# Kernel optimization log

Measured on AMD Instinct MI355X. Metric: run time of the kernel, lower is better.

Reference implementation:

```python
import jax, jax.numpy as jnp
import numpy as np


def setup_inputs() -> dict:
    key = jax.random.key(0)
    ks = jax.random.split(key, 8)
    B, W, H, C = 4, 64, 64, 256
    C2 = C // 2
    s = 0.05
    x = jax.random.normal(ks[0], (B, W, H, C), dtype=jnp.float32)
    Wq = jax.random.normal(ks[1], (C, C2), dtype=jnp.float32) * s
    bq = jax.random.normal(ks[2], (C2,), dtype=jnp.float32) * s
    Wk = jax.random.normal(ks[3], (C, C2), dtype=jnp.float32) * s
    bk = jax.random.normal(ks[4], (C2,), dtype=jnp.float32) * s
    Wv = jax.random.normal(ks[5], (C, C), dtype=jnp.float32) * s
    bv = jax.random.normal(ks[6], (C,), dtype=jnp.float32) * s
    # gamma is initialized to 0 in the original; use a nonzero value so the
    # attention branch actually contributes (math is identical).
    gamma = jnp.array([0.5], dtype=jnp.float32)
    return {"x": x, "Wq": Wq, "bq": bq, "Wk": Wk, "bk": bk, "Wv": Wv, "bv": bv, "gamma": gamma}


def reference(x, Wq, bq, Wk, bk, Wv, bv, gamma):
    B, W, H, C = x.shape
    N = W * H
    # 1x1 convs == per-pixel linear projections
    q = jnp.einsum('bwhc,cd->bwhd', x, Wq) + bq   # [B,W,H,C/2]
    k = jnp.einsum('bwhc,cd->bwhd', x, Wk) + bk   # [B,W,H,C/2]
    v = jnp.einsum('bwhc,cd->bwhd', x, Wv) + bv   # [B,W,H,C]
    # Faithful to original: raw row-major reshape (B,W,H,Cq) -> (B,Cq,N)
    # (this mixes spatial and channel axes, exactly as the TF code does)
    pq = q.reshape(B, -1, N)                      # [B,C/2,N]
    pk = k.reshape(B, -1, N)                      # [B,C/2,N]
    pv = v.reshape(B, -1, N)                      # [B,C,N]
    energy = jnp.einsum('bcn,bcm->bnm', pq, pk)   # [B,N,N] (pq transposed)
    attention = jax.nn.softmax(energy, axis=-1)   # [B,N,N]
    out = jnp.einsum('bcm,bnm->bcn', pv, attention)  # pv @ attention^T
    out = out.reshape(B, W, H, C)
    return gamma * out + x
```

## Files before the change

kernel.cpp:

```cpp
#include <hip/hip_runtime.h>
#include <hip/hip_bf16.h>
#include <stdint.h>


typedef __attribute__((ext_vector_type(8)))  short short8;
typedef __attribute__((ext_vector_type(4)))  float f32x4;
typedef __attribute__((ext_vector_type(16))) float f32x16;
typedef __attribute__((ext_vector_type(4)))  unsigned short u16x4;

#define MFMA16 __builtin_amdgcn_mfma_f32_16x16x32_bf16
#define MFMA32 __builtin_amdgcn_mfma_f32_32x32x16_bf16

__device__ __forceinline__ unsigned short f2bf(float f) {
    union { float f; uint32_t u; } v; v.f = f;
    return (unsigned short)((v.u + 0x8000u) >> 16);
}
__device__ __forceinline__ float bf2f(unsigned short h) {
    union { uint32_t u; float f; } v; v.u = ((uint32_t)h) << 16;
    return v.f;
}
__device__ __forceinline__ uint32_t pkbf(float a, float b) {
    union { __hip_bfloat162 h; uint32_t u; } v;
    v.h = __float22bfloat162_rn(float2{a, b});
    return v.u;
}

__global__ void prep_w(const float* __restrict__ Wq, const float* __restrict__ bq,
                       const float* __restrict__ Wk, const float* __restrict__ bk,
                       const float* __restrict__ Wv, const float* __restrict__ bv,
                       unsigned short* __restrict__ Wt, float* __restrict__ bias) {
    int g = blockIdx.x * 256 + threadIdx.x;
    int c = g & 255, d = g >> 8;
    float val;
    if (d < 128)      val = Wq[c * 128 + d];
    else if (d < 256) val = Wk[c * 128 + (d - 128)];
    else              val = Wv[c * 256 + (d - 256)];
    Wt[d * 256 + c] = f2bf(val);
    if (g < 512) {
        float bb;
        if (g < 128)      bb = bq[g];
        else if (g < 256) bb = bk[g - 128];
        else              bb = bv[g - 256];
        bias[g] = bb;
    }
}

__global__ __launch_bounds__(256) void proj(
        const float* __restrict__ x, const unsigned short* __restrict__ Wt,
        const float* __restrict__ bias,
        unsigned short* __restrict__ Qrm, unsigned short* __restrict__ Krm,
        unsigned short* __restrict__ Vbf) {
    __shared__ unsigned short T[128 * 136];
    int bid = blockIdx.x;
    int tid = threadIdx.x;
    int wave = tid >> 6, lane = tid & 63;
    int l16 = lane & 15, quad = lane >> 4;

    int kind, b, a, vh = 0;
    if (bid < 256) { kind = bid >> 7; int s = bid & 127; b = s >> 5; a = s & 31; }
    else           { kind = 2; int s = bid - 256; vh = s >> 7; b = (s >> 5) & 3; a = s & 31; }

    short8 af[2][8];
    #pragma unroll
    for (int g = 0; g < 2; ++g) {
        int p_local = wave * 32 + g * 16 + l16;
        int pix = (kind == 2) ? (b * 4096 + a * 128 + p_local)
                              : (b * 4096 + a + 32 * p_local);
        const float* xr = x + (size_t)pix * 256;
        #pragma unroll
        for (int kk = 0; kk < 8; ++kk) {
            f32x4 u0 = *(const f32x4*)(xr + kk * 32 + quad * 8);
            f32x4 u1 = *(const f32x4*)(xr + kk * 32 + quad * 8 + 4);
            union { short8 s; uint32_t u[4]; } h;
            h.u[0] = pkbf(u0[0], u0[1]); h.u[1] = pkbf(u0[2], u0[3]);
            h.u[2] = pkbf(u1[0], u1[1]); h.u[3] = pkbf(u1[2], u1[3]);
            af[g][kk] = h.s;
        }
    }

    if (kind < 2) {
        int dbase = kind * 128;
        unsigned short* out = kind ? Krm : Qrm;
        #pragma unroll 1
        for (int dt = 0; dt < 8; ++dt) {
            int d = dbase + dt * 16 + l16;
            float bval = bias[d];
            f32x4 acc0 = {0.f,0.f,0.f,0.f}, acc1 = {0.f,0.f,0.f,0.f};
            #pragma unroll
            for (int kk = 0; kk < 8; ++kk) {
                short8 wrow = *(const short8*)(Wt + d * 256 + kk * 32 + quad * 8);
                acc0 = MFMA16(af[0][kk], wrow, acc0, 0, 0, 0);
                acc1 = MFMA16(af[1][kk], wrow, acc1, 0, 0, 0);
            }
            #pragma unroll
            for (int g = 0; g < 2; ++g) {
                f32x4 acc = g ? acc1 : acc0;
                union { u16x4 v; uint32_t u[2]; } pk;
                pk.u[0] = pkbf(acc[0] + bval, acc[1] + bval);
                pk.u[1] = pkbf(acc[2] + bval, acc[3] + bval);
                *(u16x4*)(T + (dt * 16 + l16) * 136 + wave * 32 + g * 16 + quad * 4) = pk.v;
            }
        }
        __syncthreads();
        unsigned short* ob = out + (b << 19) + a * 128 * 128;
        #pragma unroll
        for (int it = 0; it < 8; ++it) {
            int ci = it * 256 + tid;
            int row = ci >> 4, cj = ci & 15;
            *(short8*)(ob + row * 128 + cj * 8) = *(const short8*)(T + row * 136 + cj * 8);
        }
    } else {
        #pragma unroll 1
        for (int dt = 0; dt < 8; ++dt) {
            int d = 256 + vh * 128 + dt * 16 + l16;
            f32x4 acc0 = {0.f,0.f,0.f,0.f}, acc1 = {0.f,0.f,0.f,0.f};
            #pragma unroll
            for (int kk = 0; kk < 8; ++kk) {
                short8 wrow = *(const short8*)(Wt + d * 256 + kk * 32 + quad * 8);
                acc0 = MFMA16(wrow, af[0][kk], acc0, 0, 0, 0);
                acc1 = MFMA16(wrow, af[1][kk], acc1, 0, 0, 0);
            }
            int dvl = dt * 16 + quad * 4;
            f32x4 bv4 = *(const f32x4*)(bias + 256 + vh * 128 + dvl);
            #pragma unroll
            for (int g = 0; g < 2; ++g) {
                f32x4 acc = g ? acc1 : acc0;
                union { u16x4 v; uint32_t u[2]; } pk;
                pk.u[0] = pkbf(acc[0] + bv4[0], acc[1] + bv4[1]);
                pk.u[1] = pkbf(acc[2] + bv4[2], acc[3] + bv4[3]);
                int p_local = wave * 32 + g * 16 + l16;
                *(u16x4*)(T + p_local * 136 + dvl) = pk.v;
            }
        }
        __syncthreads();
        #pragma unroll
        for (int it = 0; it < 8; ++it) {
            int cid = it * 256 + tid;
            int c_local = cid >> 8, w = cid & 255;
            int p_local = c_local * 16 + (w >> 4);
            int m = (w >> 4) * 256 + vh * 128 + (w & 15) * 8;
            *(short8*)(Vbf + (b << 20) + (size_t)(a * 8 + c_local) * 4096 + m)
                = *(const short8*)(T + p_local * 136 + (w & 15) * 8);
        }
    }
}

__global__ __launch_bounds__(256, 2) void attn(
        const unsigned short* __restrict__ Qrm, const unsigned short* __restrict__ Krm,
        const unsigned short* __restrict__ Vbf, unsigned short* __restrict__ Opart,
        float* __restrict__ Lpart) {
    __shared__ unsigned short Vs[256 * 72];
    __shared__ unsigned short Ps[64 * 72];

    int bid = blockIdx.x;
    int comb = bid & 7, qt = bid >> 3;
    int b = comb >> 1, ks = comb & 1;
    int tid = threadIdx.x, wave = tid >> 6, lane = tid & 63;
    int l32 = lane & 31, half = lane >> 5;
    int mt = wave & 1, nt = wave >> 1;

    const unsigned short* Qb = Qrm + (b << 19);
    const unsigned short* Kb = Krm + (b << 19);
    const unsigned short* Vb = Vbf + (b << 20);

    int q0 = qt * 64;

    short8 qf[8];
    {
        const unsigned short* qrow = Qb + (q0 + nt * 32 + l32) * 128 + half * 8;
        #pragma unroll
        for (int kk = 0; kk < 8; ++kk) qf[kk] = *(const short8*)(qrow + kk * 16);
    }

    f32x16 O[2][2];
    #pragma unroll
    for (int i = 0; i < 2; ++i)
        #pragma unroll
        for (int j = 0; j < 2; ++j)
            #pragma unroll
            for (int r = 0; r < 16; ++r) O[i][j][r] = 0.f;
    float l_run = 0.f;

    const int m_base = ks * 2048;
    int vrow = tid >> 3, vch = tid & 7;

    short8 vreg[8];
    #pragma unroll
    for (int i = 0; i < 8; ++i)
        vreg[i] = *(const short8*)(Vb + (size_t)(vrow + i * 32) * 4096 + m_base + vch * 8);
    short8 kf[8];
    {
        const unsigned short* krow = Kb + (m_base + mt * 32 + l32) * 128 + half * 8;
        #pragma unroll
        for (int kk = 0; kk < 8; ++kk) kf[kk] = *(const short8*)(krow + kk * 16);
    }

    #pragma unroll 1
    for (int kt = 0; kt < 32; ++kt) {
        __syncthreads();
        #pragma unroll
        for (int i = 0; i < 8; ++i)
            *(short8*)(Vs + (vrow + i * 32) * 72 + vch * 8) = vreg[i];

        f32x16 S;
        #pragma unroll
        for (int r = 0; r < 16; ++r) S[r] = 0.f;
        #pragma unroll
        for (int kk = 0; kk < 8; ++kk) S = MFMA32(kf[kk], qf[kk], S, 0, 0, 0);

        #pragma unroll
        for (int g = 0; g < 4; ++g) {
            float p0 = __expf(S[g * 4 + 0]), p1 = __expf(S[g * 4 + 1]);
            float p2 = __expf(S[g * 4 + 2]), p3 = __expf(S[g * 4 + 3]);
            l_run += (p0 + p1) + (p2 + p3);
            union { u16x4 v; uint32_t u[2]; } pk;
            pk.u[0] = pkbf(p0, p1); pk.u[1] = pkbf(p2, p3);
            *(u16x4*)(Ps + (nt * 32 + l32) * 72 + mt * 32 + g * 8 + half * 4) = pk.v;
        }

        __syncthreads();

        if (kt < 31) {
            int m1 = m_base + (kt + 1) * 64;
            #pragma unroll
            for (int i = 0; i < 8; ++i)
                vreg[i] = *(const short8*)(Vb + (size_t)(vrow + i * 32) * 4096 + m1 + vch * 8);
            const unsigned short* krow = Kb + (m1 + mt * 32 + l32) * 128 + half * 8;
            #pragma unroll
            for (int kk = 0; kk < 8; ++kk) kf[kk] = *(const short8*)(krow + kk * 16);
        }

        #pragma unroll
        for (int k2 = 0; k2 < 4; ++k2) {
            short8 pa0 = *(const short8*)(Ps + (l32) * 72 + k2 * 16 + half * 8);
            short8 pa1 = *(const short8*)(Ps + (32 + l32) * 72 + k2 * 16 + half * 8);
            #pragma unroll
            for (int c2 = 0; c2 < 2; ++c2) {
                short8 vb = *(const short8*)(Vs + ((wave * 2 + c2) * 32 + l32) * 72 + k2 * 16 + half * 8);
                O[0][c2] = MFMA32(pa0, vb, O[0][c2], 0, 0, 0);
                O[1][c2] = MFMA32(pa1, vb, O[1][c2], 0, 0, 0);
            }
        }
    }

    l_run += __shfl_xor(l_run, 32);
    unsigned short* Op = Opart + ((size_t)(ks * 4 + b) << 20);
    #pragma unroll
    for (int q2 = 0; q2 < 2; ++q2)
        #pragma unroll
        for (int c2 = 0; c2 < 2; ++c2) {
            int c = (wave * 2 + c2) * 32 + l32;
            #pragma unroll
            for (int r = 0; r < 16; ++r) {
                int n = q0 + q2 * 32 + (r & 3) + 8 * (r >> 2) + 4 * half;
                Op[(size_t)n * 256 + c] = f2bf(O[q2][c2][r]);
            }
        }
    if (half == 0) {
        int n = q0 + nt * 32 + l32;
        Lpart[((ks * 2 + mt) * 4 + b) * 4096 + n] = l_run;
    }
}

__global__ __launch_bounds__(256) void merge_out(
        const unsigned short* __restrict__ Opart, const float* __restrict__ Lpart,
        const float* __restrict__ x, const float* __restrict__ gamma,
        float* __restrict__ out) {
    __shared__ float tile[64][65];
    __shared__ float wsm[64];
    int b  = blockIdx.x >> 6;
    int n0 = (blockIdx.x & 63) << 6;
    int tid = threadIdx.x;
    float g = gamma[0];
    if (tid < 64) {
        int n = n0 + tid;
        float L = 0.f;
        #pragma unroll
        for (int s = 0; s < 4; ++s) L += Lpart[(s * 4 + b) * 4096 + n];
        wsm[tid] = g / L;
    }
    __syncthreads();
    int cl  = tid & 63, nl4 = tid >> 6;
    int nl  = tid & 63, cl4 = tid >> 6;
    for (int cc = 0; cc < 4; ++cc) {
        for (int i = 0; i < 16; ++i) {
            int n = n0 + i * 4 + nl4;
            int c = (cc << 6) + cl;
            float On = 0.f;
            #pragma unroll
            for (int s = 0; s < 2; ++s)
                On += bf2f(Opart[((size_t)(s * 4 + b) << 20) + (size_t)n * 256 + c]);
            tile[cl][i * 4 + nl4] = On * wsm[i * 4 + nl4];
        }
        __syncthreads();
        for (int j = 0; j < 16; ++j) {
            int c = (cc << 6) + j * 4 + cl4;
            int idx = (b << 20) + c * 4096 + n0 + nl;
            out[idx] = tile[j * 4 + cl4][nl] + x[idx];
        }
        __syncthreads();
    }
}

extern "C" void kernel_launch(void* const* d_in, const int* in_sizes, int n_in,
                              void* d_out, int out_size, void* d_ws, size_t ws_size,
                              hipStream_t stream) {
    const float* x     = (const float*)d_in[0];
    const float* Wq    = (const float*)d_in[1];
    const float* bq    = (const float*)d_in[2];
    const float* Wk    = (const float*)d_in[3];
    const float* bk    = (const float*)d_in[4];
    const float* Wv    = (const float*)d_in[5];
    const float* bv    = (const float*)d_in[6];
    const float* gamma = (const float*)d_in[7];
    float* out = (float*)d_out;

    if (ws_size < 34080768u) return;

    char* ws = (char*)d_ws;
    unsigned short* Wt    = (unsigned short*)(ws);
    float*          bias  = (float*)        (ws +   262144);
    unsigned short* Qrm   = (unsigned short*)(ws +   264192);
    unsigned short* Krm   = (unsigned short*)(ws +  4458496);
    unsigned short* Vbf   = (unsigned short*)(ws +  8652800);
    unsigned short* Opart = (unsigned short*)(ws + 17041408);
    float*          Lpart = (float*)        (ws + 33818624);

    prep_w   <<<512, 256, 0, stream>>>(Wq, bq, Wk, bk, Wv, bv, Wt, bias);
    proj     <<<512, 256, 0, stream>>>(x, Wt, bias, Qrm, Krm, Vbf);
    attn     <<<512, 256, 0, stream>>>(Qrm, Krm, Vbf, Opart, Lpart);
    merge_out<<<256, 256, 0, stream>>>(Opart, Lpart, x, gamma, out);
}
```

Measured before the change: 194.9 us.

## Repack K and V into fragment-chunked layouts and load V fragments directly

The projection kernel now writes K and V in chunked layouts, 16 elements per row per chunk, so each MFMA fragment is a contiguous 32-byte load. The attention kernel drops the shared-memory V staging and loads V fragments straight from global memory into registers. P is double-buffered in LDS, which removes one barrier per iteration. merge_out is rewritten to use vectorized bf16 loads, a single 64x256 transposed tile and float4 stores. This trades LDS traffic and syncs for more global and L2 fragment loads, and adds register pressure from the 8 V fragments held per wave.

```diff
diff --git a/kernel.cpp b/kernel.cpp
--- a/kernel.cpp
+++ b/kernel.cpp
@@ -48,8 +48,8 @@
 __global__ __launch_bounds__(256) void proj(
         const float* __restrict__ x, const unsigned short* __restrict__ Wt,
         const float* __restrict__ bias,
-        unsigned short* __restrict__ Qrm, unsigned short* __restrict__ Krm,
-        unsigned short* __restrict__ Vbf) {
+        unsigned short* __restrict__ Qrm, unsigned short* __restrict__ Kp,
+        unsigned short* __restrict__ Vp) {
     __shared__ unsigned short T[128 * 136];
     int bid = blockIdx.x;
     int tid = threadIdx.x;
@@ -80,7 +80,6 @@
 
     if (kind < 2) {
         int dbase = kind * 128;
-        unsigned short* out = kind ? Krm : Qrm;
         #pragma unroll 1
         for (int dt = 0; dt < 8; ++dt) {
             int d = dbase + dt * 16 + l16;
@@ -102,12 +101,23 @@
             }
         }
         __syncthreads();
-        unsigned short* ob = out + (b << 19) + a * 128 * 128;
-        #pragma unroll
-        for (int it = 0; it < 8; ++it) {
-            int ci = it * 256 + tid;
-            int row = ci >> 4, cj = ci & 15;
-            *(short8*)(ob + row * 128 + cj * 8) = *(const short8*)(T + row * 136 + cj * 8);
+        if (kind == 0) {
+            unsigned short* ob = Qrm + (b << 19) + a * 128 * 128;
+            #pragma unroll
+            for (int it = 0; it < 8; ++it) {
+                int ci = it * 256 + tid;
+                int row = ci >> 4, cj = ci & 15;
+                *(short8*)(ob + row * 128 + cj * 8) = *(const short8*)(T + row * 136 + cj * 8);
+            }
+        } else {
+            unsigned short* kb = Kp + (b << 19);
+            #pragma unroll
+            for (int it = 0; it < 8; ++it) {
+                int ci = it * 256 + tid;
+                int row = ci >> 4, cj = ci & 15;
+                *(short8*)(kb + (cj >> 1) * 65536 + (a * 128 + row) * 16 + (cj & 1) * 8)
+                    = *(const short8*)(T + row * 136 + cj * 8);
+            }
         }
     } else {
         #pragma unroll 1
@@ -133,24 +143,24 @@
             }
         }
         __syncthreads();
+        unsigned short* vb = Vp + (b << 20);
         #pragma unroll
         for (int it = 0; it < 8; ++it) {
             int cid = it * 256 + tid;
             int c_local = cid >> 8, w = cid & 255;
             int p_local = c_local * 16 + (w >> 4);
-            int m = (w >> 4) * 256 + vh * 128 + (w & 15) * 8;
-            *(short8*)(Vbf + (b << 20) + (size_t)(a * 8 + c_local) * 4096 + m)
+            int chunk = (w >> 4) * 16 + vh * 8 + ((w & 15) >> 1);
+            *(short8*)(vb + chunk * 4096 + (a * 8 + c_local) * 16 + (w & 1) * 8)
                 = *(const short8*)(T + p_local * 136 + (w & 15) * 8);
         }
     }
 }
 
 __global__ __launch_bounds__(256, 2) void attn(
-        const unsigned short* __restrict__ Qrm, const unsigned short* __restrict__ Krm,
-        const unsigned short* __restrict__ Vbf, unsigned short* __restrict__ Opart,
+        const unsigned short* __restrict__ Qrm, const unsigned short* __restrict__ Kp,
+        const unsigned short* __restrict__ Vp, unsigned short* __restrict__ Opart,
         float* __restrict__ Lpart) {
-    __shared__ unsigned short Vs[256 * 72];
-    __shared__ unsigned short Ps[64 * 72];
+    __shared__ unsigned short Ps[2 * 64 * 72];
 
     int bid = blockIdx.x;
     int comb = bid & 7, qt = bid >> 3;
@@ -160,8 +170,8 @@
     int mt = wave & 1, nt = wave >> 1;
 
     const unsigned short* Qb = Qrm + (b << 19);
-    const unsigned short* Kb = Krm + (b << 19);
-    const unsigned short* Vb = Vbf + (b << 20);
+    const unsigned short* Kb = Kp + (b << 19);
+    const unsigned short* Vb = Vp + (b << 20);
 
     int q0 = qt * 64;
 
@@ -182,25 +192,24 @@
     float l_run = 0.f;
 
     const int m_base = ks * 2048;
-    int vrow = tid >> 3, vch = tid & 7;
-
-    short8 vreg[8];
-    #pragma unroll
-    for (int i = 0; i < 8; ++i)
-        vreg[i] = *(const short8*)(Vb + (size_t)(vrow + i * 32) * 4096 + m_base + vch * 8);
+    const int chunk_base = ks * 128;
+
+    int krow = (m_base + mt * 32 + l32) * 16 + half * 8;
     short8 kf[8];
-    {
-        const unsigned short* krow = Kb + (m_base + mt * 32 + l32) * 128 + half * 8;
-        #pragma unroll
-        for (int kk = 0; kk < 8; ++kk) kf[kk] = *(const short8*)(krow + kk * 16);
-    }
+    #pragma unroll
+    for (int kk = 0; kk < 8; ++kk)
+        kf[kk] = *(const short8*)(Kb + kk * 65536 + krow);
+    short8 vfrag[2][4];
+    #pragma unroll
+    for (int c2 = 0; c2 < 2; ++c2)
+        #pragma unroll
+        for (int k2 = 0; k2 < 4; ++k2)
+            vfrag[c2][k2] = *(const short8*)(Vb + (chunk_base + k2) * 4096
+                              + ((wave * 2 + c2) * 32 + l32) * 16 + half * 8);
 
     #pragma unroll 1
     for (int kt = 0; kt < 32; ++kt) {
-        __syncthreads();
-        #pragma unroll
-        for (int i = 0; i < 8; ++i)
-            *(short8*)(Vs + (vrow + i * 32) * 72 + vch * 8) = vreg[i];
+        unsigned short* Pb = Ps + (kt & 1) * (64 * 72);
 
         f32x16 S;
         #pragma unroll
@@ -215,31 +224,36 @@
             l_run += (p0 + p1) + (p2 + p3);
             union { u16x4 v; uint32_t u[2]; } pk;
             pk.u[0] = pkbf(p0, p1); pk.u[1] = pkbf(p2, p3);
-            *(u16x4*)(Ps + (nt * 32 + l32) * 72 + mt * 32 + g * 8 + half * 4) = pk.v;
+            *(u16x4*)(Pb + (nt * 32 + l32) * 72 + mt * 32 + g * 8 + half * 4) = pk.v;
         }
 
         __syncthreads();
 
         if (kt < 31) {
-            int m1 = m_base + (kt + 1) * 64;
-            #pragma unroll
-            for (int i = 0; i < 8; ++i)
-                vreg[i] = *(const short8*)(Vb + (size_t)(vrow + i * 32) * 4096 + m1 + vch * 8);
-            const unsigned short* krow = Kb + (m1 + mt * 32 + l32) * 128 + half * 8;
-            #pragma unroll
-            for (int kk = 0; kk < 8; ++kk) kf[kk] = *(const short8*)(krow + kk * 16);
+            int kr1 = (m_base + (kt + 1) * 64 + mt * 32 + l32) * 16 + half * 8;
+            #pragma unroll
+            for (int kk = 0; kk < 8; ++kk)
+                kf[kk] = *(const short8*)(Kb + kk * 65536 + kr1);
         }
 
         #pragma unroll
         for (int k2 = 0; k2 < 4; ++k2) {
-            short8 pa0 = *(const short8*)(Ps + (l32) * 72 + k2 * 16 + half * 8);
-            short8 pa1 = *(const short8*)(Ps + (32 + l32) * 72 + k2 * 16 + half * 8);
-            #pragma unroll
-            for (int c2 = 0; c2 < 2; ++c2) {
-                short8 vb = *(const short8*)(Vs + ((wave * 2 + c2) * 32 + l32) * 72 + k2 * 16 + half * 8);
-                O[0][c2] = MFMA32(pa0, vb, O[0][c2], 0, 0, 0);
-                O[1][c2] = MFMA32(pa1, vb, O[1][c2], 0, 0, 0);
-            }
+            short8 pa0 = *(const short8*)(Pb + (l32) * 72 + k2 * 16 + half * 8);
+            short8 pa1 = *(const short8*)(Pb + (32 + l32) * 72 + k2 * 16 + half * 8);
+            O[0][0] = MFMA32(pa0, vfrag[0][k2], O[0][0], 0, 0, 0);
+            O[0][1] = MFMA32(pa0, vfrag[1][k2], O[0][1], 0, 0, 0);
+            O[1][0] = MFMA32(pa1, vfrag[0][k2], O[1][0], 0, 0, 0);
+            O[1][1] = MFMA32(pa1, vfrag[1][k2], O[1][1], 0, 0, 0);
+        }
+
+        if (kt < 31) {
+            int ch1 = chunk_base + (kt + 1) * 4;
+            #pragma unroll
+            for (int c2 = 0; c2 < 2; ++c2)
+                #pragma unroll
+                for (int k2 = 0; k2 < 4; ++k2)
+                    vfrag[c2][k2] = *(const short8*)(Vb + (ch1 + k2) * 4096
+                                      + ((wave * 2 + c2) * 32 + l32) * 16 + half * 8);
         }
     }
 
@@ -266,7 +280,7 @@
         const unsigned short* __restrict__ Opart, const float* __restrict__ Lpart,
         const float* __restrict__ x, const float* __restrict__ gamma,
         float* __restrict__ out) {
-    __shared__ float tile[64][65];
+    __shared__ float tile[64 * 257];
     __shared__ float wsm[64];
     int b  = blockIdx.x >> 6;
     int n0 = (blockIdx.x & 63) << 6;
@@ -280,25 +294,32 @@
         wsm[tid] = g / L;
     }
     __syncthreads();
-    int cl  = tid & 63, nl4 = tid >> 6;
-    int nl  = tid & 63, cl4 = tid >> 6;
-    for (int cc = 0; cc < 4; ++cc) {
-        for (int i = 0; i < 16; ++i) {
-            int n = n0 + i * 4 + nl4;
-            int c = (cc << 6) + cl;
-            float On = 0.f;
-            #pragma unroll
-            for (int s = 0; s < 2; ++s)
-                On += bf2f(Opart[((size_t)(s * 4 + b) << 20) + (size_t)n * 256 + c]);
-            tile[cl][i * 4 + nl4] = On * wsm[i * 4 + nl4];
-        }
-        __syncthreads();
-        for (int j = 0; j < 16; ++j) {
-            int c = (cc << 6) + j * 4 + cl4;
-            int idx = (b << 20) + c * 4096 + n0 + nl;
-            out[idx] = tile[j * 4 + cl4][nl] + x[idx];
-        }
-        __syncthreads();
+    int nl1 = tid >> 5, cb1 = (tid & 31) * 8;
+    const unsigned short* Op0 = Opart + ((size_t)(0 * 4 + b) << 20);
+    const unsigned short* Op1 = Opart + ((size_t)(1 * 4 + b) << 20);
+    #pragma unroll
+    for (int i = 0; i < 8; ++i) {
+        int nl = i * 8 + nl1;
+        size_t off = (size_t)(n0 + nl) * 256 + cb1;
+        short8 o0 = *(const short8*)(Op0 + off);
+        short8 o1 = *(const short8*)(Op1 + off);
+        float w = wsm[nl];
+        float* tr = tile + nl * 257 + cb1;
+        #pragma unroll
+        for (int e = 0; e < 8; ++e)
+            tr[e] = (bf2f((unsigned short)o0[e]) + bf2f((unsigned short)o1[e])) * w;
+    }
+    __syncthreads();
+    int cg = tid >> 4, nq = (tid & 15) * 4;
+    #pragma unroll
+    for (int it = 0; it < 16; ++it) {
+        int c = it * 16 + cg;
+        size_t idx = ((size_t)b << 20) + (size_t)c * 4096 + n0 + nq;
+        f32x4 xv = *(const f32x4*)(x + idx);
+        f32x4 ov;
+        #pragma unroll
+        for (int e = 0; e < 4; ++e) ov[e] = tile[(nq + e) * 257 + c] + xv[e];
+        *(f32x4*)(out + idx) = ov;
     }
 }
 
@@ -321,13 +342,13 @@
     unsigned short* Wt    = (unsigned short*)(ws);
     float*          bias  = (float*)        (ws +   262144);
     unsigned short* Qrm   = (unsigned short*)(ws +   264192);
-    unsigned short* Krm   = (unsigned short*)(ws +  4458496);
-    unsigned short* Vbf   = (unsigned short*)(ws +  8652800);
+    unsigned short* Kp    = (unsigned short*)(ws +  4458496);
+    unsigned short* Vp    = (unsigned short*)(ws +  8652800);
     unsigned short* Opart = (unsigned short*)(ws + 17041408);
     float*          Lpart = (float*)        (ws + 33818624);
 
     prep_w   <<<512, 256, 0, stream>>>(Wq, bq, Wk, bk, Wv, bv, Wt, bias);
-    proj     <<<512, 256, 0, stream>>>(x, Wt, bias, Qrm, Krm, Vbf);
-    attn     <<<512, 256, 0, stream>>>(Qrm, Krm, Vbf, Opart, Lpart);
+    proj     <<<512, 256, 0, stream>>>(x, Wt, bias, Qrm, Kp, Vp);
+    attn     <<<512, 256, 0, stream>>>(Qrm, Kp, Vp, Opart, Lpart);
     merge_out<<<256, 256, 0, stream>>>(Opart, Lpart, x, gamma, out);
 }
```

New measurement: 175.4 us. 10.0% less time.
